# Performance work log

Measured on AMD Instinct MI355X. Metric: run time of the kernel, lower is better.

Reference implementation:

```python
import jax, jax.numpy as jnp
import numpy as np

K = 3
SIGMA = 1.0


def setup_inputs() -> dict:
    key = jax.random.key(0)
    k1, k2 = jax.random.split(key)
    B, N = 32, 1024
    predictions = jax.random.normal(k1, (B, N), dtype=jnp.float32)
    # integer relevance grades 0..4, stored as float as in the torch module
    relevance_scores = jax.random.randint(k2, (B, N), 0, 5).astype(jnp.float32)
    return {"predictions": predictions, "relevance_scores": relevance_scores}


def reference(predictions, relevance_scores):
    B, N = predictions.shape
    dt = predictions.dtype

    # lambda weights: rows and columns of top-k predicted items get doubled.
    # weight[b,i,j] = 2^{m[b,i]} * 2^{m[b,j]} with m the top-k membership mask
    _, topk_idx = jax.lax.top_k(predictions, K)  # [B, K]
    m = jnp.zeros((B, N), dtype=dt).at[jnp.arange(B)[:, None], topk_idx].set(1.0)
    mult = 1.0 + m  # 2^m for m in {0,1}
    lambda_weights = mult[:, :, None] * mult[:, None, :]  # [B, N, N]

    pred_diff = predictions[:, :, None] - predictions[:, None, :]  # [B, N, N]
    rel_diff = relevance_scores[:, :, None] - relevance_scores[:, None, :]

    targets = (rel_diff > 0).astype(dt)
    x = SIGMA * pred_diff
    # BCE-with-logits: softplus(x) - t*x  (numerically stable)
    pairwise_loss = jax.nn.softplus(x) - targets * x

    valid_pairs = (rel_diff != 0).astype(dt)
    weighted = pairwise_loss * lambda_weights * valid_pairs
    num_valid = valid_pairs.sum(axis=(1, 2)) + 1e-8
    loss = weighted.sum(axis=(1, 2)) / num_valid
    return loss.mean()
```

## Files before the change

kernel.cpp:

```cpp
#include <hip/hip_runtime.h>
#include <math.h>

#define NN 1024
#define BTH 256
#define NT 16
#define NTILES 136
#define TBLK 34
#define BPB (TBLK + 1)

#define OFF_T 0
#define OFF_C 17408
#define OFF_V 17536
#define OFF_L 17664
#define OFF_CB 17792
#define OFF_CG 21888

__device__ __forceinline__ float pair_f(float pi, float ri, float pj, float rj) {
    const float x = pi - pj;
    const float y = (ri > rj) ? -x : x;
    const float e = __expf(-fabsf(y));
    const float f = fmaxf(y, 0.0f) + __logf(1.0f + e);
    return (ri != rj) ? f : 0.0f;
}

__device__ __forceinline__ void sinkf(float v) { asm volatile("" :: "v"(v)); }

__global__ void __launch_bounds__(BTH)
fused_kernel(const float* __restrict__ pred, const float* __restrict__ rel,
             char* __restrict__ ws, float* __restrict__ out, int B) {
    const int t = threadIdx.x;
    const int w = t >> 6, l = t & 63;
    const int blk = blockIdx.x;

    __shared__ float  s_p[NN];
    __shared__ float  s_r[NN];
    __shared__ float2 s_seg[4][64];
    __shared__ float  s_rv[3][4];
    __shared__ int    s_ri[3][4];
    __shared__ int    s_hist[4][5];
    __shared__ float  s_red[4];
    __shared__ float  s_corr, s_cnt;
    __shared__ int    s_flag, s_flag2;

    float* slotT = (float*)(ws + OFF_T);
    float* slotC = (float*)(ws + OFF_C);
    float* slotV = (float*)(ws + OFF_V);
    float* lossS = (float*)(ws + OFF_L);

    int b;
    if (blk < B) {
        b = blk;
        const size_t base = (size_t)b * NN;
        const float4 p4 = ((const float4*)(pred + base))[t];
        const float4 r4 = ((const float4*)(rel  + base))[t];
        ((float4*)s_p)[t] = p4;
        ((float4*)s_r)[t] = r4;

        for (int g = 0; g < 5; ++g) {
            const float gf = (float)g;
            int c = __popcll(__ballot(r4.x == gf)) + __popcll(__ballot(r4.y == gf))
                  + __popcll(__ballot(r4.z == gf)) + __popcll(__ballot(r4.w == gf));
            if (l == 0) s_hist[w][g] = c;
        }

        int w1 = -1, w2 = -1, w3 = -1;
        const int n0 = t * 4;
        for (int k = 0; k < 3; ++k) {
            float bv = -INFINITY;
            int   bi = NN;
            if (n0 + 0 != w1 && n0 + 0 != w2 && p4.x > bv) { bv = p4.x; bi = n0 + 0; }
            if (n0 + 1 != w1 && n0 + 1 != w2 && p4.y > bv) { bv = p4.y; bi = n0 + 1; }
            if (n0 + 2 != w1 && n0 + 2 != w2 && p4.z > bv) { bv = p4.z; bi = n0 + 2; }
            if (n0 + 3 != w1 && n0 + 3 != w2 && p4.w > bv) { bv = p4.w; bi = n0 + 3; }
            for (int off = 32; off > 0; off >>= 1) {
                const float ov = __shfl_xor(bv, off);
                const int   oi = __shfl_xor(bi, off);
                if (ov > bv || (ov == bv && oi < bi)) { bv = ov; bi = oi; }
            }
            if (l == 0) { s_rv[k][w] = bv; s_ri[k][w] = bi; }
            __syncthreads();
            bv = s_rv[k][0]; bi = s_ri[k][0];
            for (int q = 1; q < 4; ++q) {
                const float ov = s_rv[k][q]; const int oi = s_ri[k][q];
                if (ov > bv || (ov == bv && oi < bi)) { bv = ov; bi = oi; }
            }
            if (k == 0) w1 = bi; else if (k == 1) w2 = bi; else w3 = bi;
        }

        float part = 0.0f;
        for (int k = 0; k < 3; ++k) {
            const int row = (k == 0) ? w1 : (k == 1) ? w2 : w3;
            const float pk = s_p[row], rk = s_r[row];
#pragma unroll
            for (int c = 0; c < 4; ++c) {
                const int j = t + c * BTH;
                part += pair_f(pk, rk, s_p[j], s_r[j]);
            }
        }
        for (int off = 32; off > 0; off >>= 1) part += __shfl_down(part, off);
        if (l == 0) s_red[w] = part;
        __syncthreads();
        if (t == 0) {
            const float R = s_red[0] + s_red[1] + s_red[2] + s_red[3];
            const float TT = 2.0f * (pair_f(s_p[w1], s_r[w1], s_p[w2], s_r[w2])
                                   + pair_f(s_p[w1], s_r[w1], s_p[w3], s_r[w3])
                                   + pair_f(s_p[w2], s_r[w2], s_p[w3], s_r[w3]));
            atomicExch(&slotC[b], 2.0f * R + TT);
            int s2 = 0;
            for (int g = 0; g < 5; ++g) {
                const int cg = s_hist[0][g] + s_hist[1][g] + s_hist[2][g] + s_hist[3][g];
                s2 += cg * cg;
            }
            atomicExch(&slotV[b], (float)(NN * NN - s2));
        }
    } else {
        const int idx = blk - B;
        b = idx / TBLK;
        const int L = (idx % TBLK) * 4 + w;
        int rem = L, ti = 0;
        while (rem >= NT - ti) { rem -= NT - ti; ++ti; }
        const int tj = ti + rem;
        const size_t base = (size_t)b * NN;
        const int i0 = ti * 64, j0 = tj * 64;

        const float jp = pred[base + j0 + l];
        const float jr = rel [base + j0 + l];
        s_seg[w][l] = make_float2(pred[base + i0 + l], rel[base + i0 + l]);

        float a = 0.0f;
        if (ti != tj) {
#pragma unroll 16
            for (int ii = 0; ii < 64; ++ii) {
                const float2 v = s_seg[w][ii];
                a += pair_f(v.x, v.y, jp, jr);
            }
        } else {
#pragma unroll 16
            for (int ii = 0; ii < 64; ++ii) {
                const float2 v = s_seg[w][ii];
                const float f = pair_f(v.x, v.y, jp, jr);
                a += (l > ii) ? f : 0.0f;
            }
        }
        for (int off = 32; off > 0; off >>= 1) a += __shfl_down(a, off);
        if (l == 0)
            atomicExch(&slotT[(size_t)b * NTILES + L], 2.0f * a);
    }

    __syncthreads();
    if (t == 0) {
        unsigned int* ctr_b = (unsigned int*)(ws + OFF_CB + (size_t)b * 128);
        const unsigned int old = atomicInc(ctr_b, (unsigned int)(BPB - 1));
        s_flag = (old == (unsigned int)(BPB - 2)) ? 1 : 0;
    }
    __syncthreads();
    if (!s_flag) return;

    {
        float v = 0.0f;
        if (t < NTILES)            v = atomicAdd(&slotT[(size_t)b * NTILES + t], 0.0f);
        else if (t == NTILES)      s_corr = atomicAdd(&slotC[b], 0.0f);
        else if (t == NTILES + 1)  s_cnt  = atomicAdd(&slotV[b], 0.0f);
        for (int off = 32; off > 0; off >>= 1) v += __shfl_down(v, off);
        if (l == 0) s_red[w] = v;
        __syncthreads();
        if (t == 0) {
            const float S = s_red[0] + s_red[1] + s_red[2] + s_red[3];
            const float loss_b = (S + s_corr) / (s_cnt + 1e-8f);
            sinkf(atomicExch(&lossS[b], loss_b));
            unsigned int* ctrG = (unsigned int*)(ws + OFF_CG);
            const unsigned int o2 = atomicInc(ctrG, (unsigned int)(B - 1));
            s_flag2 = (o2 == (unsigned int)(B - 2)) ? 1 : 0;
        }
        __syncthreads();
        if (s_flag2 && w == 0) {
            float u = (l < B) ? atomicAdd(&lossS[l], 0.0f) : 0.0f;
            for (int off = 32; off > 0; off >>= 1) u += __shfl_down(u, off);
            if (l == 0) out[0] = u / (float)B;
        }
    }
}

extern "C" void kernel_launch(void* const* d_in, const int* in_sizes, int n_in,
                              void* d_out, int out_size, void* d_ws, size_t ws_size,
                              hipStream_t stream) {
    const float* pred = (const float*)d_in[0];
    const float* rel  = (const float*)d_in[1];
    float* out = (float*)d_out;

    const int B = in_sizes[0] / NN;

    fused_kernel<<<B + TBLK * B, BTH, 0, stream>>>(pred, rel, (char*)d_ws, out, B);
}
```

Before: 21.70 us.

## Use 512-thread blocks and single-pass top-3 merge reduction

Doubles the block size to 512 threads and halves the number of tile blocks per batch row, so each block handles eight 64x64 tiles instead of four. The top-k selection now keeps a running top-3 list per lane and merges the lists through wave shuffles and one shared-memory pass, replacing three sequential argmax rounds that each needed a block barrier. This cuts barriers and launched blocks, and the final-block counter sees fewer arrivals. In exchange the grid has fewer, larger blocks, which may lower occupancy and the number of CUs kept busy.

```diff
diff --git a/kernel.cpp b/kernel.cpp
--- a/kernel.cpp
+++ b/kernel.cpp
@@ -2,10 +2,10 @@
 #include <math.h>
 
 #define NN 1024
-#define BTH 256
+#define BTH 512
 #define NT 16
 #define NTILES 136
-#define TBLK 34
+#define TBLK 17
 #define BPB (TBLK + 1)
 
 #define OFF_T 0
@@ -25,6 +25,17 @@
 
 __device__ __forceinline__ void sinkf(float v) { asm volatile("" :: "v"(v)); }
 
+__device__ __forceinline__ bool better(float v, int i, float V, int I) {
+    return (v > V) || (v == V && i < I);
+}
+__device__ __forceinline__ void ins3(float x, int ix,
+                                     float& a1, int& i1, float& a2, int& i2,
+                                     float& a3, int& i3) {
+    if (better(x, ix, a1, i1))      { a3=a2; i3=i2; a2=a1; i2=i1; a1=x; i1=ix; }
+    else if (better(x, ix, a2, i2)) { a3=a2; i3=i2; a2=x;  i2=ix; }
+    else if (better(x, ix, a3, i3)) { a3=x;  i3=ix; }
+}
+
 __global__ void __launch_bounds__(BTH)
 fused_kernel(const float* __restrict__ pred, const float* __restrict__ rel,
              char* __restrict__ ws, float* __restrict__ out, int B) {
@@ -34,11 +45,11 @@
 
     __shared__ float  s_p[NN];
     __shared__ float  s_r[NN];
-    __shared__ float2 s_seg[4][64];
-    __shared__ float  s_rv[3][4];
-    __shared__ int    s_ri[3][4];
-    __shared__ int    s_hist[4][5];
-    __shared__ float  s_red[4];
+    __shared__ float2 s_seg[8][64];
+    __shared__ float  s_tv[8][3];
+    __shared__ int    s_ti[8][3];
+    __shared__ int    s_hist[8][5];
+    __shared__ float  s_red[8];
     __shared__ float  s_corr, s_cnt;
     __shared__ int    s_flag, s_flag2;
 
@@ -51,64 +62,68 @@
     if (blk < B) {
         b = blk;
         const size_t base = (size_t)b * NN;
-        const float4 p4 = ((const float4*)(pred + base))[t];
-        const float4 r4 = ((const float4*)(rel  + base))[t];
-        ((float4*)s_p)[t] = p4;
-        ((float4*)s_r)[t] = r4;
+        const float2 p2 = ((const float2*)(pred + base))[t];
+        const float2 r2 = ((const float2*)(rel  + base))[t];
+        ((float2*)s_p)[t] = p2;
+        ((float2*)s_r)[t] = r2;
 
         for (int g = 0; g < 5; ++g) {
             const float gf = (float)g;
-            int c = __popcll(__ballot(r4.x == gf)) + __popcll(__ballot(r4.y == gf))
-                  + __popcll(__ballot(r4.z == gf)) + __popcll(__ballot(r4.w == gf));
+            const int c = __popcll(__ballot(r2.x == gf)) + __popcll(__ballot(r2.y == gf));
             if (l == 0) s_hist[w][g] = c;
         }
 
-        int w1 = -1, w2 = -1, w3 = -1;
-        const int n0 = t * 4;
-        for (int k = 0; k < 3; ++k) {
-            float bv = -INFINITY;
-            int   bi = NN;
-            if (n0 + 0 != w1 && n0 + 0 != w2 && p4.x > bv) { bv = p4.x; bi = n0 + 0; }
-            if (n0 + 1 != w1 && n0 + 1 != w2 && p4.y > bv) { bv = p4.y; bi = n0 + 1; }
-            if (n0 + 2 != w1 && n0 + 2 != w2 && p4.z > bv) { bv = p4.z; bi = n0 + 2; }
-            if (n0 + 3 != w1 && n0 + 3 != w2 && p4.w > bv) { bv = p4.w; bi = n0 + 3; }
-            for (int off = 32; off > 0; off >>= 1) {
-                const float ov = __shfl_xor(bv, off);
-                const int   oi = __shfl_xor(bi, off);
-                if (ov > bv || (ov == bv && oi < bi)) { bv = ov; bi = oi; }
-            }
-            if (l == 0) { s_rv[k][w] = bv; s_ri[k][w] = bi; }
-            __syncthreads();
-            bv = s_rv[k][0]; bi = s_ri[k][0];
-            for (int q = 1; q < 4; ++q) {
-                const float ov = s_rv[k][q]; const int oi = s_ri[k][q];
-                if (ov > bv || (ov == bv && oi < bi)) { bv = ov; bi = oi; }
-            }
-            if (k == 0) w1 = bi; else if (k == 1) w2 = bi; else w3 = bi;
-        }
+        const int n0 = t * 2;
+        float a1, a2, a3; int i1, i2, i3;
+        if (p2.y > p2.x) { a1 = p2.y; i1 = n0 + 1; a2 = p2.x; i2 = n0; }
+        else             { a1 = p2.x; i1 = n0;     a2 = p2.y; i2 = n0 + 1; }
+        a3 = -INFINITY; i3 = NN;
+
+        for (int off = 32; off > 0; off >>= 1) {
+            const float b1 = __shfl_xor(a1, off), b2 = __shfl_xor(a2, off),
+                        b3 = __shfl_xor(a3, off);
+            const int   j1 = __shfl_xor(i1, off), j2 = __shfl_xor(i2, off),
+                        j3 = __shfl_xor(i3, off);
+            ins3(b1, j1, a1, i1, a2, i2, a3, i3);
+            ins3(b2, j2, a1, i1, a2, i2, a3, i3);
+            ins3(b3, j3, a1, i1, a2, i2, a3, i3);
+        }
+        if (l == 0) {
+            s_tv[w][0] = a1; s_tv[w][1] = a2; s_tv[w][2] = a3;
+            s_ti[w][0] = i1; s_ti[w][1] = i2; s_ti[w][2] = i3;
+        }
+        __syncthreads();
+
+        float c1 = s_tv[0][0], c2 = s_tv[0][1], c3 = s_tv[0][2];
+        int   d1 = s_ti[0][0], d2 = s_ti[0][1], d3 = s_ti[0][2];
+        for (int q = 1; q < 8; ++q) {
+            ins3(s_tv[q][0], s_ti[q][0], c1, d1, c2, d2, c3, d3);
+            ins3(s_tv[q][1], s_ti[q][1], c1, d1, c2, d2, c3, d3);
+            ins3(s_tv[q][2], s_ti[q][2], c1, d1, c2, d2, c3, d3);
+        }
+        const int w1 = d1, w2 = d2, w3 = d3;
 
         float part = 0.0f;
         for (int k = 0; k < 3; ++k) {
             const int row = (k == 0) ? w1 : (k == 1) ? w2 : w3;
             const float pk = s_p[row], rk = s_r[row];
-#pragma unroll
-            for (int c = 0; c < 4; ++c) {
-                const int j = t + c * BTH;
-                part += pair_f(pk, rk, s_p[j], s_r[j]);
-            }
+            part += pair_f(pk, rk, s_p[t],       s_r[t]);
+            part += pair_f(pk, rk, s_p[t + BTH], s_r[t + BTH]);
         }
         for (int off = 32; off > 0; off >>= 1) part += __shfl_down(part, off);
         if (l == 0) s_red[w] = part;
         __syncthreads();
         if (t == 0) {
-            const float R = s_red[0] + s_red[1] + s_red[2] + s_red[3];
+            float R = 0.0f;
+            for (int q = 0; q < 8; ++q) R += s_red[q];
             const float TT = 2.0f * (pair_f(s_p[w1], s_r[w1], s_p[w2], s_r[w2])
                                    + pair_f(s_p[w1], s_r[w1], s_p[w3], s_r[w3])
                                    + pair_f(s_p[w2], s_r[w2], s_p[w3], s_r[w3]));
             atomicExch(&slotC[b], 2.0f * R + TT);
             int s2 = 0;
             for (int g = 0; g < 5; ++g) {
-                const int cg = s_hist[0][g] + s_hist[1][g] + s_hist[2][g] + s_hist[3][g];
+                int cg = 0;
+                for (int q = 0; q < 8; ++q) cg += s_hist[q][g];
                 s2 += cg * cg;
             }
             atomicExch(&slotV[b], (float)(NN * NN - s2));
@@ -116,7 +131,7 @@
     } else {
         const int idx = blk - B;
         b = idx / TBLK;
-        const int L = (idx % TBLK) * 4 + w;
+        const int L = (idx % TBLK) * 8 + w;
         int rem = L, ti = 0;
         while (rem >= NT - ti) { rem -= NT - ti; ++ti; }
         const int tj = ti + rem;
@@ -165,7 +180,8 @@
         if (l == 0) s_red[w] = v;
         __syncthreads();
         if (t == 0) {
-            const float S = s_red[0] + s_red[1] + s_red[2] + s_red[3];
+            float S = 0.0f;
+            for (int q = 0; q < 8; ++q) S += s_red[q];
             const float loss_b = (S + s_corr) / (s_cnt + 1e-8f);
             sinkf(atomicExch(&lossS[b], loss_b));
             unsigned int* ctrG = (unsigned int*)(ws + OFF_CG);
```

After: 28.05 us. 1.29x slower.
